# Kernel tuning notes

Measured on AMD Instinct MI355X. Metric: run time of the kernel, lower is better.

The kernel has to match this reference:

```python
import jax, jax.numpy as jnp
import numpy as np

N, D = 8192, 128
BATCH_SIZE = 8192  # init kwarg; final loss divisor
EPS = 1e-12        # F.normalize eps


def _normalize(x):
    n = jnp.maximum(jnp.linalg.norm(x, axis=-1, keepdims=True), EPS)
    return x / n


def _alignment(x, y, alpha=2.0):
    # (x - y).norm(p=2, dim=1).pow(2).mean() == mean of squared row diffs
    return jnp.mean(jnp.sum((x - y) ** 2, axis=1))


def _uniformity(x, t=2.0):
    # torch.pdist(x).pow(2) == squared euclidean distance for all i<j pairs.
    # Use gram-matrix identity; mask to strict upper triangle.
    n = x.shape[0]
    sq = jnp.sum(x * x, axis=1)                      # [N]
    d2 = sq[:, None] + sq[None, :] - 2.0 * (x @ x.T)  # [N, N]
    d2 = jnp.maximum(d2, 0.0)
    iu = jnp.triu(jnp.ones((n, n), dtype=bool), k=1)
    num_pairs = n * (n - 1) // 2
    mean_val = jnp.sum(jnp.where(iu, jnp.exp(-t * d2), 0.0)) / num_pairs
    return jnp.log(mean_val)


def setup_inputs() -> dict:
    key = jax.random.key(0)
    k1, k2, k3 = jax.random.split(key, 3)
    return {
        "users": jax.random.normal(k1, (N, D), dtype=jnp.float32),
        "pos_items": jax.random.normal(k2, (N, D), dtype=jnp.float32),
        "neg_items": jax.random.normal(k3, (N, D), dtype=jnp.float32),
    }


def reference(users, pos_items, neg_items):
    # neg_items is accepted but unused, matching the original forward.
    user_n = _normalize(users)
    item_n = _normalize(pos_items)
    align = _alignment(user_n, item_n)
    uniform = 0.5 * (_uniformity(user_n) + _uniformity(item_n)) / 2.0
    loss = (align + uniform) / BATCH_SIZE
    return loss
```

## Files before the change

### kernel.cpp

```cpp
#include <hip/hip_runtime.h>
#include <hip/hip_bf16.h>

typedef __bf16 bf16x8 __attribute__((ext_vector_type(8)));
typedef float  f32x4  __attribute__((ext_vector_type(4)));

#define NROWS 8192
#define DIM   128
#define NB    64
#define JOBS_PER_MAT 2080

__device__ __forceinline__ float waveReduceSum(float v) {
    for (int off = 32; off; off >>= 1) v += __shfl_xor(v, off, 64);
    return v;
}

__device__ __forceinline__ float fast_exp2(float x) {
    return __builtin_amdgcn_exp2f(x);
}

__device__ __forceinline__ void gload16(const void* g, void* l) {
    __builtin_amdgcn_global_load_lds(
        (const __attribute__((address_space(1))) unsigned int*)(uintptr_t)g,
        (__attribute__((address_space(3))) unsigned int*)(uintptr_t)l,
        16, 0, 0);
}

__device__ __forceinline__ int tri(int b) { return b * NB - (b * (b - 1)) / 2; }

__global__ __launch_bounds__(256) void prep_kernel(
    const float* __restrict__ users, const float* __restrict__ pos,
    __bf16* __restrict__ Uh, __bf16* __restrict__ Ph,
    double* __restrict__ alignPart)
{
    const int tid  = threadIdx.x;
    const int lane = tid & 63;
    const int w    = tid >> 6;
    const int l32  = lane & 31;
    const int half = lane >> 5;
    const int r    = blockIdx.x * 8 + w * 2 + half;

    const float4 u4 = ((const float4*)users)[r * 32 + l32];
    const float4 p4 = ((const float4*)pos )[r * 32 + l32];

    float su = u4.x*u4.x + u4.y*u4.y + u4.z*u4.z + u4.w*u4.w;
    float sp = p4.x*p4.x + p4.y*p4.y + p4.z*p4.z + p4.w*p4.w;
    for (int off = 16; off; off >>= 1) {
        su += __shfl_xor(su, off, 64);
        sp += __shfl_xor(sp, off, 64);
    }
    const float nu  = fmaxf(sqrtf(su), 1e-12f);
    const float npp = fmaxf(sqrtf(sp), 1e-12f);

    const float ux = u4.x / nu,  uy = u4.y / nu,  uz = u4.z / nu,  uw = u4.w / nu;
    const float px = p4.x / npp, py = p4.y / npp, pz = p4.z / npp, pw = p4.w / npp;

    union { __bf16 h[4]; uint2 q; } cu, cp;
    cu.h[0] = (__bf16)ux; cu.h[1] = (__bf16)uy; cu.h[2] = (__bf16)uz; cu.h[3] = (__bf16)uw;
    cp.h[0] = (__bf16)px; cp.h[1] = (__bf16)py; cp.h[2] = (__bf16)pz; cp.h[3] = (__bf16)pw;
    ((uint2*)Uh)[r * 32 + l32] = cu.q;
    ((uint2*)Ph)[r * 32 + l32] = cp.q;

    const float dx = ux - px, dy = uy - py, dz = uz - pz, dw = uw - pw;
    float al = dx*dx + dy*dy + dz*dz + dw*dw;
    for (int off = 16; off; off >>= 1) al += __shfl_xor(al, off, 64);
    al += __shfl_xor(al, 32, 64);

    __shared__ float wsum[4];
    if (lane == 0) wsum[w] = al;
    __syncthreads();
    if (tid == 0)
        alignPart[blockIdx.x] = (double)wsum[0] + (double)wsum[1]
                              + (double)wsum[2] + (double)wsum[3];
}

__global__ __launch_bounds__(256, 4) void gram_kernel(
    const __bf16* __restrict__ Uh, const __bf16* __restrict__ Ph,
    double* __restrict__ Spart)
{
    __shared__ __align__(16) unsigned char smem[32768];
    __shared__ float wsum[4];

    const int bid = blockIdx.x;
    const int mat = bid >= JOBS_PER_MAT;
    const int t   = bid - (mat ? JOBS_PER_MAT : 0);

    int bi = (int)((NB + 0.5f) - sqrtf((NB + 0.5f) * (NB + 0.5f) - 2.0f * (float)t));
    if (bi > 0 && tri(bi) > t) --bi;
    if (tri(bi + 1) <= t) ++bi;
    const int bj = bi + (t - tri(bi));

    const char* __restrict__ Xb = (const char*)(mat ? Ph : Uh);

    const int tid  = threadIdx.x;
    const int lane = tid & 63;
    const int w    = tid >> 6;

    const int r0 = w * 32 + (lane >> 3);
    const int gcOff = (((lane & 7) ^ (r0 & 7)) << 4);
    const char* gA0 = Xb + (size_t)(bi * 128 + r0) * 256 + gcOff;
    const char* gB0 = Xb + (size_t)(bj * 128 + r0) * 256 + gcOff;
    unsigned char* lA0 = smem + w * 4096;

#define STAGE(h)                                                           \
    {                                                                      \
        const int hb = (h) * 128;                                          \
        _Pragma("unroll")                                                  \
        for (int i_ = 0; i_ < 4; ++i_) {                                   \
            gload16(gA0 + hb + i_ * 2048, lA0 + i_ * 1024);                \
            gload16(gB0 + hb + i_ * 2048, lA0 + 16384 + i_ * 1024);        \
        }                                                                  \
    }

    const int wm = w >> 1, wn = w & 1;
    const int lr = lane & 15;
    const int lg = lane >> 4;
    const unsigned cxor = (unsigned)(lr & 7);
    const unsigned aOff = (unsigned)(wm * 64 + lr) * 128;
    const unsigned bOff = (unsigned)(wn * 64 + lr) * 128 + 16384;

    f32x4 acc[4][4];
#pragma unroll
    for (int mi = 0; mi < 4; ++mi)
#pragma unroll
        for (int ni = 0; ni < 4; ++ni)
            acc[mi][ni] = (f32x4){0.f, 0.f, 0.f, 0.f};

#define COMPUTE                                                             \
    {                                                                       \
        _Pragma("unroll")                                                   \
        for (int ks2 = 0; ks2 < 2; ++ks2) {                                 \
            const unsigned sc = (((unsigned)(ks2 * 4 + lg)) ^ cxor) << 4;   \
            bf16x8 a[4], b[4];                                              \
            _Pragma("unroll")                                               \
            for (int mi = 0; mi < 4; ++mi)                                  \
                a[mi] = *reinterpret_cast<const bf16x8*>(                   \
                    smem + aOff + mi * 2048 + sc);                          \
            _Pragma("unroll")                                               \
            for (int ni = 0; ni < 4; ++ni)                                  \
                b[ni] = *reinterpret_cast<const bf16x8*>(                   \
                    smem + bOff + ni * 2048 + sc);                          \
            _Pragma("unroll")                                               \
            for (int mi = 0; mi < 4; ++mi)                                  \
                _Pragma("unroll")                                           \
                for (int ni = 0; ni < 4; ++ni)                              \
                    acc[mi][ni] = __builtin_amdgcn_mfma_f32_16x16x32_bf16(  \
                        a[mi], b[ni], acc[mi][ni], 0, 0, 0);                \
        }                                                                   \
    }

    STAGE(0)
    __syncthreads();
    COMPUTE
    __syncthreads();
    STAGE(1)
    __syncthreads();
    COMPUTE

    const float C1 = 4.0f * 1.4426950408889634f;
    float s0 = 0.f, s1 = 0.f, s2 = 0.f, s3 = 0.f;
#pragma unroll
    for (int mi = 0; mi < 4; ++mi)
#pragma unroll
        for (int ni = 0; ni < 4; ++ni) {
            const f32x4 v = acc[mi][ni];
            s0 += fast_exp2(v[0] * C1 - C1);
            s1 += fast_exp2(v[1] * C1 - C1);
            s2 += fast_exp2(v[2] * C1 - C1);
            s3 += fast_exp2(v[3] * C1 - C1);
        }

    const float s = waveReduceSum((s0 + s1) + (s2 + s3));
    if (lane == 0) wsum[w] = s;
    __syncthreads();
    if (tid == 0) {
        double bs = (double)wsum[0] + (double)wsum[1]
                  + (double)wsum[2] + (double)wsum[3];
        if (bi != bj) bs *= 2.0;
        Spart[bid] = bs;
    }
#undef STAGE
#undef COMPUTE
}

__global__ __launch_bounds__(1024) void finalize_kernel(
    const double* __restrict__ alignPart, const double* __restrict__ Spart,
    float* __restrict__ out)
{
    const int tid = threadIdx.x;
    double a = 0.0, su = 0.0, sp = 0.0;
    for (int i = tid; i < 1024; i += 1024) a += alignPart[i];
    for (int i = tid; i < 2 * JOBS_PER_MAT; i += 1024) {
        const double v = Spart[i];
        if (i < JOBS_PER_MAT) su += v; else sp += v;
    }
    for (int off = 32; off; off >>= 1) {
        a  += __shfl_xor(a,  off, 64);
        su += __shfl_xor(su, off, 64);
        sp += __shfl_xor(sp, off, 64);
    }
    __shared__ double sh[3][16];
    const int lane = tid & 63, wid = tid >> 6;
    if (lane == 0) { sh[0][wid] = a; sh[1][wid] = su; sh[2][wid] = sp; }
    __syncthreads();
    if (tid == 0) {
        double A = 0.0, SU = 0.0, SP = 0.0;
        for (int i = 0; i < 16; ++i) { A += sh[0][i]; SU += sh[1][i]; SP += sh[2][i]; }
        const double Nd = 8192.0;
        const double npairs = Nd * (Nd - 1.0) * 0.5;
        const double align = A / Nd;
        const double mu = (SU - Nd) * 0.5 / npairs;
        const double mp = (SP - Nd) * 0.5 / npairs;
        const double uniform = 0.25 * (log(mu) + log(mp));
        out[0] = (float)((align + uniform) / 8192.0);
    }
}

extern "C" void kernel_launch(void* const* d_in, const int* in_sizes, int n_in,
                              void* d_out, int out_size, void* d_ws, size_t ws_size,
                              hipStream_t stream)
{
    const float* users = (const float*)d_in[0];
    const float* pos   = (const float*)d_in[1];
    float* out = (float*)d_out;

    char* ws = (char*)d_ws;
    __bf16* Uh = (__bf16*)ws;
    __bf16* Ph = (__bf16*)(ws + 2097152);
    double* alignPart = (double*)(ws + 4194304);
    double* Spart     = (double*)(ws + 4194304 + 8192);

    hipLaunchKernelGGL(prep_kernel, dim3(1024), dim3(256), 0, stream,
                       users, pos, Uh, Ph, alignPart);
    hipLaunchKernelGGL(gram_kernel, dim3(2 * JOBS_PER_MAT), dim3(256), 0, stream,
                       Uh, Ph, Spart);
    hipLaunchKernelGGL(finalize_kernel, dim3(1), dim3(1024), 0, stream,
                       alignPart, Spart, out);
}
```

Before: 38.38 us.

## Use 32x32x16 MFMA with A operands in registers and single-stage B in LDS

Restructures the gram tile kernel so that each wave loads its A rows straight from global memory into registers. Only the B tile (128x128 bf16, 32 KB) is staged in LDS, in one pass with an XOR swizzle, and the two-phase stage/compute with its extra barriers is dropped. The inner product switches from 16x16x32 to 32x32x16 MFMA, which cuts the number of LDS fragment reads per FLOP. The cost is higher register pressure, so launch bounds drop to 3 blocks per CU, and the direct global A loads are not coalesced through LDS.

```diff
diff --git a/kernel.cpp b/kernel.cpp
--- a/kernel.cpp
+++ b/kernel.cpp
@@ -2,7 +2,7 @@
 #include <hip/hip_bf16.h>
 
 typedef __bf16 bf16x8 __attribute__((ext_vector_type(8)));
-typedef float  f32x4  __attribute__((ext_vector_type(4)));
+typedef float  f32x16 __attribute__((ext_vector_type(16)));
 
 #define NROWS 8192
 #define DIM   128
@@ -73,7 +73,7 @@
                               + (double)wsum[2] + (double)wsum[3];
 }
 
-__global__ __launch_bounds__(256, 4) void gram_kernel(
+__global__ __launch_bounds__(256, 3) void gram_kernel(
     const __bf16* __restrict__ Uh, const __bf16* __restrict__ Ph,
     double* __restrict__ Spart)
 {
@@ -94,79 +94,71 @@
     const int tid  = threadIdx.x;
     const int lane = tid & 63;
     const int w    = tid >> 6;
-
-    const int r0 = w * 32 + (lane >> 3);
-    const int gcOff = (((lane & 7) ^ (r0 & 7)) << 4);
-    const char* gA0 = Xb + (size_t)(bi * 128 + r0) * 256 + gcOff;
-    const char* gB0 = Xb + (size_t)(bj * 128 + r0) * 256 + gcOff;
-    unsigned char* lA0 = smem + w * 4096;
-
-#define STAGE(h)                                                           \
-    {                                                                      \
-        const int hb = (h) * 128;                                          \
-        _Pragma("unroll")                                                  \
-        for (int i_ = 0; i_ < 4; ++i_) {                                   \
-            gload16(gA0 + hb + i_ * 2048, lA0 + i_ * 1024);                \
-            gload16(gB0 + hb + i_ * 2048, lA0 + 16384 + i_ * 1024);        \
-        }                                                                  \
-    }
-
     const int wm = w >> 1, wn = w & 1;
-    const int lr = lane & 15;
-    const int lg = lane >> 4;
-    const unsigned cxor = (unsigned)(lr & 7);
-    const unsigned aOff = (unsigned)(wm * 64 + lr) * 128;
-    const unsigned bOff = (unsigned)(wn * 64 + lr) * 128 + 16384;
-
-    f32x4 acc[4][4];
-#pragma unroll
-    for (int mi = 0; mi < 4; ++mi)
-#pragma unroll
-        for (int ni = 0; ni < 4; ++ni)
-            acc[mi][ni] = (f32x4){0.f, 0.f, 0.f, 0.f};
-
-#define COMPUTE                                                             \
-    {                                                                       \
-        _Pragma("unroll")                                                   \
-        for (int ks2 = 0; ks2 < 2; ++ks2) {                                 \
-            const unsigned sc = (((unsigned)(ks2 * 4 + lg)) ^ cxor) << 4;   \
-            bf16x8 a[4], b[4];                                              \
-            _Pragma("unroll")                                               \
-            for (int mi = 0; mi < 4; ++mi)                                  \
-                a[mi] = *reinterpret_cast<const bf16x8*>(                   \
-                    smem + aOff + mi * 2048 + sc);                          \
-            _Pragma("unroll")                                               \
-            for (int ni = 0; ni < 4; ++ni)                                  \
-                b[ni] = *reinterpret_cast<const bf16x8*>(                   \
-                    smem + bOff + ni * 2048 + sc);                          \
-            _Pragma("unroll")                                               \
-            for (int mi = 0; mi < 4; ++mi)                                  \
-                _Pragma("unroll")                                           \
-                for (int ni = 0; ni < 4; ++ni)                              \
-                    acc[mi][ni] = __builtin_amdgcn_mfma_f32_16x16x32_bf16(  \
-                        a[mi], b[ni], acc[mi][ni], 0, 0, 0);                \
-        }                                                                   \
-    }
-
-    STAGE(0)
-    __syncthreads();
-    COMPUTE
-    __syncthreads();
-    STAGE(1)
-    __syncthreads();
-    COMPUTE
+    const int l32 = lane & 31;
+    const int lh  = lane >> 5;
+
+    const int srow  = tid >> 4;
+    const int schnk = (tid & 15) ^ srow;
+    const char* gB0 = Xb + (size_t)(bj * 128 + srow) * 256 + schnk * 16;
+    unsigned char* lB0 = smem + w * 1024;
+
+#pragma unroll
+    for (int p = 0; p < 8; ++p)
+        gload16(gB0 + p * 4096, lB0 + p * 4096);
+
+    const char* aBase = Xb + (size_t)(bi * 128 + wm * 64 + l32) * 256 + lh * 16;
+    bf16x8 a[2][8];
+#pragma unroll
+    for (int mi = 0; mi < 2; ++mi)
+#pragma unroll
+        for (int ks = 0; ks < 8; ++ks)
+            a[mi][ks] = *reinterpret_cast<const bf16x8*>(
+                aBase + mi * 32 * 256 + ks * 32);
+
+    f32x16 acc[2][2];
+#pragma unroll
+    for (int mi = 0; mi < 2; ++mi)
+#pragma unroll
+        for (int ni = 0; ni < 2; ++ni)
+#pragma unroll
+            for (int e = 0; e < 16; ++e)
+                acc[mi][ni][e] = 0.f;
+
+    __syncthreads();
+
+    const unsigned r0B = (unsigned)(wn * 64 + l32);
+#pragma unroll
+    for (int ks = 0; ks < 8; ++ks) {
+        bf16x8 b[2];
+#pragma unroll
+        for (int ni = 0; ni < 2; ++ni) {
+            const unsigned R = r0B + ni * 32;
+            const unsigned c = ((unsigned)(ks * 2 + lh)) ^ (R & 15u);
+            b[ni] = *reinterpret_cast<const bf16x8*>(smem + R * 256 + (c << 4));
+        }
+#pragma unroll
+        for (int mi = 0; mi < 2; ++mi)
+#pragma unroll
+            for (int ni = 0; ni < 2; ++ni)
+                acc[mi][ni] = __builtin_amdgcn_mfma_f32_32x32x16_bf16(
+                    a[mi][ks], b[ni], acc[mi][ni], 0, 0, 0);
+    }
 
     const float C1 = 4.0f * 1.4426950408889634f;
     float s0 = 0.f, s1 = 0.f, s2 = 0.f, s3 = 0.f;
 #pragma unroll
-    for (int mi = 0; mi < 4; ++mi)
-#pragma unroll
-        for (int ni = 0; ni < 4; ++ni) {
-            const f32x4 v = acc[mi][ni];
-            s0 += fast_exp2(v[0] * C1 - C1);
-            s1 += fast_exp2(v[1] * C1 - C1);
-            s2 += fast_exp2(v[2] * C1 - C1);
-            s3 += fast_exp2(v[3] * C1 - C1);
+    for (int mi = 0; mi < 2; ++mi)
+#pragma unroll
+        for (int ni = 0; ni < 2; ++ni) {
+            const f32x16 v = acc[mi][ni];
+#pragma unroll
+            for (int e = 0; e < 16; e += 4) {
+                s0 += fast_exp2(v[e + 0] * C1 - C1);
+                s1 += fast_exp2(v[e + 1] * C1 - C1);
+                s2 += fast_exp2(v[e + 2] * C1 - C1);
+                s3 += fast_exp2(v[e + 3] * C1 - C1);
+            }
         }
 
     const float s = waveReduceSum((s0 + s1) + (s2 + s3));
@@ -178,8 +170,6 @@
         if (bi != bj) bs *= 2.0;
         Spart[bid] = bs;
     }
-#undef STAGE
-#undef COMPUTE
 }
 
 __global__ __launch_bounds__(1024) void finalize_kernel(
```

Measured after the change: 54.00 us. +40.7%, slower.
